# Kernel tuning notes

Measured on AMD Instinct MI355X. Metric: run time of the kernel, lower is better.

## Reference

```python
import jax, jax.numpy as jnp
import numpy as np

B, T, D = 256, 512, 256

def setup_inputs() -> dict:
    key = jax.random.key(0)
    k1, k2, k3, k4 = jax.random.split(key, 4)
    ip = jax.random.normal(k1, (B, T, D), dtype=jnp.float32)
    W = jax.random.normal(k2, (D, D), dtype=jnp.float32) * (1.0 / np.sqrt(D))
    b = jax.random.normal(k3, (D,), dtype=jnp.float32) * 0.05
    context = jax.random.normal(k4, (D, 1), dtype=jnp.float32) * 0.05
    return {"ip": ip, "W": W, "b": b, "context": context}

def reference(ip, W, b, context) -> jnp.ndarray:
    # linear -> tanh: [B, T, D]
    h = jnp.tanh(jnp.einsum("btd,ed->bte", ip, W) + b)
    # attention scores over words: [B, T]
    scores = jnp.einsum("btd,d->bt", h, context[:, 0])
    attn = jax.nn.softmax(scores, axis=1)
    # weighted sum over words -> sentence embeddings: [B, D]
    sent_embeds = jnp.einsum("bt,btd->bd", attn, ip)
    return sent_embeds
```

## Files before the change

### kernel.cpp

```cpp
#include <hip/hip_runtime.h>
#include <hip/hip_bf16.h>

#define NBATCH 256
#define NT 512
#define ND 256
#define NROWS (NBATCH * NT)

typedef __attribute__((ext_vector_type(8))) short short8;
typedef __attribute__((ext_vector_type(4))) float floatx4;

__device__ __forceinline__ unsigned short f2bf(float x) {
    unsigned int u = __float_as_uint(x);
    u += 0x7FFFu + ((u >> 16) & 1u);
    return (unsigned short)(u >> 16);
}

__global__ void __launch_bounds__(256) prep_kernel(
    const float* __restrict__ W, unsigned short* __restrict__ wf)
{
    int g  = blockIdx.x * 256 + threadIdx.x;
    int m  = g & 15, q = (g >> 4) & 3, s = (g >> 6) & 7, nb = g >> 9;
    const float* src = W + (nb * 16 + m) * ND + q * 8 + s * 32;
    float4 f0 = *(const float4*)src;
    float4 f1 = *(const float4*)(src + 4);
    short8 v;
    v[0] = (short)f2bf(f0.x); v[1] = (short)f2bf(f0.y);
    v[2] = (short)f2bf(f0.z); v[3] = (short)f2bf(f0.w);
    v[4] = (short)f2bf(f1.x); v[5] = (short)f2bf(f1.y);
    v[6] = (short)f2bf(f1.z); v[7] = (short)f2bf(f1.w);
    *(short8*)(wf + (long)g * 8) = v;
}

__global__ void __launch_bounds__(256, 4) scores_kernel(
    const float* __restrict__ ip,
    const unsigned short* __restrict__ wf,
    const float* __restrict__ bias,
    const float* __restrict__ ctx,
    float* __restrict__ scores)
{
    __shared__ __align__(16) char wsm[32768];
    short8* lds16 = (short8*)wsm;

    const int tid  = threadIdx.x;
    const int lane = tid & 63;
    const int wv   = tid >> 6;
    const int m    = lane & 15;
    const int q    = lane >> 4;
    const long row0 = (long)blockIdx.x * 64 + wv * 16;

    short8 a[8];
    {
        const float* ar = ip + (row0 + m) * ND + q * 8;
        float4 raw[8];
#pragma unroll
        for (int g = 0; g < 2; ++g) {
#pragma unroll
            for (int i = 0; i < 4; ++i) {
                raw[2 * i]     = *(const float4*)(ar + (4 * g + i) * 32);
                raw[2 * i + 1] = *(const float4*)(ar + (4 * g + i) * 32 + 4);
            }
#pragma unroll
            for (int i = 0; i < 4; ++i) {
                short8 v;
                v[0] = (short)f2bf(raw[2 * i].x); v[1] = (short)f2bf(raw[2 * i].y);
                v[2] = (short)f2bf(raw[2 * i].z); v[3] = (short)f2bf(raw[2 * i].w);
                v[4] = (short)f2bf(raw[2 * i + 1].x); v[5] = (short)f2bf(raw[2 * i + 1].y);
                v[6] = (short)f2bf(raw[2 * i + 1].z); v[7] = (short)f2bf(raw[2 * i + 1].w);
                a[4 * g + i] = v;
            }
        }
    }

    float sc[4] = {0.f, 0.f, 0.f, 0.f};
    const short8* wchunks = (const short8*)wf;

#pragma unroll 1
    for (int stage = 0; stage < 4; ++stage) {
        if (stage) __syncthreads();
#pragma unroll
        for (int u = 0; u < 8; ++u) {
            int c = u * 256 + tid;
            lds16[c] = wchunks[stage * 2048 + c];
        }
        __syncthreads();

#pragma unroll 1
        for (int nbl = 0; nbl < 4; ++nbl) {
            const int e = (stage * 4 + nbl) * 16 + m;
            const short8* wp = lds16 + nbl * 512 + lane;
            short8 w[8];
#pragma unroll
            for (int s = 0; s < 8; ++s) w[s] = wp[s * 64];
            floatx4 acc = {0.f, 0.f, 0.f, 0.f};
#pragma unroll
            for (int s = 0; s < 8; ++s)
                acc = __builtin_amdgcn_mfma_f32_16x16x32_bf16(a[s], w[s], acc, 0, 0, 0);
            const float be  = bias[e];
            const float ce  = ctx[e];
            const float ce2 = ce + ce;
#pragma unroll
            for (int r = 0; r < 4; ++r) {
                float x = acc[r] + be;
                float t = __builtin_amdgcn_rcpf(__expf(x + x) + 1.f);
                sc[r] = __builtin_fmaf(-ce2, t, sc[r] + ce);
            }
        }
    }

#pragma unroll
    for (int off = 8; off >= 1; off >>= 1) {
#pragma unroll
        for (int r = 0; r < 4; ++r)
            sc[r] += __shfl_xor(sc[r], off, 64);
    }
    if (m == 0) {
#pragma unroll
        for (int r = 0; r < 4; ++r)
            scores[row0 + q * 4 + r] = sc[r];
    }
}

__global__ void __launch_bounds__(256) wsum_kernel(
    const float* __restrict__ ip,
    const float* __restrict__ scores,
    float* __restrict__ out)
{
    __shared__ float attn_s[NT];
    __shared__ float red[8];
    __shared__ float partial[16][64];

    const int b  = blockIdx.x >> 2;
    const int dq = blockIdx.x & 3;
    const int tid  = threadIdx.x;
    const int lane = tid & 63;
    const int wv   = tid >> 6;

    float s0 = scores[(long)b * NT + tid];
    float s1 = scores[(long)b * NT + tid + 256];
    float mx = fmaxf(s0, s1);
#pragma unroll
    for (int off = 32; off >= 1; off >>= 1) mx = fmaxf(mx, __shfl_xor(mx, off, 64));
    if (lane == 0) red[wv] = mx;
    __syncthreads();
    mx = fmaxf(fmaxf(red[0], red[1]), fmaxf(red[2], red[3]));
    float e0 = __expf(s0 - mx), e1 = __expf(s1 - mx);
    float sm = e0 + e1;
#pragma unroll
    for (int off = 32; off >= 1; off >>= 1) sm += __shfl_xor(sm, off, 64);
    __syncthreads();
    if (lane == 0) red[4 + wv] = sm;
    __syncthreads();
    sm = red[4] + red[5] + red[6] + red[7];
    float inv = 1.f / sm;
    attn_s[tid]       = e0 * inv;
    attn_s[tid + 256] = e1 * inv;
    __syncthreads();

    const int dg = tid & 15;
    const int ts = tid >> 4;
    const float4* base = (const float4*)(ip + (long)b * NT * ND + dq * 64) + dg;
    float a0 = 0.f, a1 = 0.f, a2 = 0.f, a3 = 0.f;
#pragma unroll 8
    for (int t = ts * 32; t < ts * 32 + 32; ++t) {
        float w = attn_s[t];
        float4 v = base[t * 64];
        a0 += w * v.x; a1 += w * v.y; a2 += w * v.z; a3 += w * v.w;
    }
    partial[ts][dg * 4 + 0] = a0;
    partial[ts][dg * 4 + 1] = a1;
    partial[ts][dg * 4 + 2] = a2;
    partial[ts][dg * 4 + 3] = a3;
    __syncthreads();
    if (tid < 64) {
        float r = 0.f;
#pragma unroll
        for (int i = 0; i < 16; ++i) r += partial[i][tid];
        out[(long)b * ND + dq * 64 + tid] = r;
    }
}

extern "C" void kernel_launch(void* const* d_in, const int* in_sizes, int n_in,
                              void* d_out, int out_size, void* d_ws, size_t ws_size,
                              hipStream_t stream) {
    const float* ip   = (const float*)d_in[0];
    const float* W    = (const float*)d_in[1];
    const float* bias = (const float*)d_in[2];
    const float* ctx  = (const float*)d_in[3];

    unsigned short* wf = (unsigned short*)d_ws;
    float* scores = (float*)((char*)d_ws + ND * ND * sizeof(unsigned short));

    prep_kernel<<<32, 256, 0, stream>>>(W, wf);
    scores_kernel<<<NROWS / 64, 256, 0, stream>>>(ip, wf, bias, ctx, scores);
    wsum_kernel<<<NBATCH * 4, 256, 0, stream>>>(ip, scores, (float*)d_out);
}
```

Baseline: 232.9 us.

## Fuse weighted sum into scores kernel with split-softmax partials and combine pass

The separate weighted-sum kernel, which re-read all of ip from global memory, is folded into the scores kernel. Each 64-row block now computes a local max and exp-sum, weights its own rows (still cache-hot from the MFMA load) and writes a partial 256-vector. A small combine kernel merges the 8 chunks per batch with flash-style rescaling. This removes a full second pass over the 128 MB input. The cost is extra shared-memory syncs and reductions in the main kernel plus a partial-result buffer in workspace.

```diff
diff --git a/kernel.cpp b/kernel.cpp
--- a/kernel.cpp
+++ b/kernel.cpp
@@ -5,6 +5,7 @@
 #define NT 512
 #define ND 256
 #define NROWS (NBATCH * NT)
+#define NCHUNK (NROWS / 64)
 
 typedef __attribute__((ext_vector_type(8))) short short8;
 typedef __attribute__((ext_vector_type(4))) float floatx4;
@@ -31,14 +32,17 @@
     *(short8*)(wf + (long)g * 8) = v;
 }
 
-__global__ void __launch_bounds__(256, 4) scores_kernel(
+__global__ void __launch_bounds__(256, 4) fused_kernel(
     const float* __restrict__ ip,
     const unsigned short* __restrict__ wf,
     const float* __restrict__ bias,
     const float* __restrict__ ctx,
-    float* __restrict__ scores)
+    float* __restrict__ gpart,
+    float2* __restrict__ ml)
 {
     __shared__ __align__(16) char wsm[32768];
+    __shared__ float score_s[64];
+    __shared__ float w_s[64];
     short8* lds16 = (short8*)wsm;
 
     const int tid  = threadIdx.x;
@@ -116,67 +120,73 @@
     if (m == 0) {
 #pragma unroll
         for (int r = 0; r < 4; ++r)
-            scores[row0 + q * 4 + r] = sc[r];
-    }
-}
-
-__global__ void __launch_bounds__(256) wsum_kernel(
-    const float* __restrict__ ip,
-    const float* __restrict__ scores,
-    float* __restrict__ out)
-{
-    __shared__ float attn_s[NT];
-    __shared__ float red[8];
-    __shared__ float partial[16][64];
-
-    const int b  = blockIdx.x >> 2;
-    const int dq = blockIdx.x & 3;
-    const int tid  = threadIdx.x;
-    const int lane = tid & 63;
-    const int wv   = tid >> 6;
-
-    float s0 = scores[(long)b * NT + tid];
-    float s1 = scores[(long)b * NT + tid + 256];
-    float mx = fmaxf(s0, s1);
+            score_s[wv * 16 + q * 4 + r] = sc[r];
+    }
+    __syncthreads();
+
+    float s = score_s[lane];
+    float mx = s;
 #pragma unroll
     for (int off = 32; off >= 1; off >>= 1) mx = fmaxf(mx, __shfl_xor(mx, off, 64));
-    if (lane == 0) red[wv] = mx;
+    float w = __expf(s - mx);
+    float lsum = w;
+#pragma unroll
+    for (int off = 32; off >= 1; off >>= 1) lsum += __shfl_xor(lsum, off, 64);
+    if (wv == 0) w_s[lane] = w;
+    if (tid == 0) ml[blockIdx.x] = make_float2(mx, lsum);
     __syncthreads();
-    mx = fmaxf(fmaxf(red[0], red[1]), fmaxf(red[2], red[3]));
-    float e0 = __expf(s0 - mx), e1 = __expf(s1 - mx);
-    float sm = e0 + e1;
-#pragma unroll
-    for (int off = 32; off >= 1; off >>= 1) sm += __shfl_xor(sm, off, 64);
-    __syncthreads();
-    if (lane == 0) red[4 + wv] = sm;
-    __syncthreads();
-    sm = red[4] + red[5] + red[6] + red[7];
-    float inv = 1.f / sm;
-    attn_s[tid]       = e0 * inv;
-    attn_s[tid + 256] = e1 * inv;
-    __syncthreads();
-
-    const int dg = tid & 15;
-    const int ts = tid >> 4;
-    const float4* base = (const float4*)(ip + (long)b * NT * ND + dq * 64) + dg;
-    float a0 = 0.f, a1 = 0.f, a2 = 0.f, a3 = 0.f;
-#pragma unroll 8
-    for (int t = ts * 32; t < ts * 32 + 32; ++t) {
-        float w = attn_s[t];
-        float4 v = base[t * 64];
-        a0 += w * v.x; a1 += w * v.y; a2 += w * v.z; a3 += w * v.w;
-    }
-    partial[ts][dg * 4 + 0] = a0;
-    partial[ts][dg * 4 + 1] = a1;
-    partial[ts][dg * 4 + 2] = a2;
-    partial[ts][dg * 4 + 3] = a3;
+
+    const float4* base = (const float4*)ip + ((long)blockIdx.x * 64 + wv * 16) * 64 + lane;
+    float4 acc4 = {0.f, 0.f, 0.f, 0.f};
+#pragma unroll
+    for (int r = 0; r < 16; ++r) {
+        float wt = w_s[wv * 16 + r];
+        float4 v = base[(long)r * 64];
+        acc4.x += wt * v.x; acc4.y += wt * v.y;
+        acc4.z += wt * v.z; acc4.w += wt * v.w;
+    }
+    float4* part4 = (float4*)wsm;
+    part4[wv * 64 + lane] = acc4;
     __syncthreads();
     if (tid < 64) {
-        float r = 0.f;
-#pragma unroll
-        for (int i = 0; i < 16; ++i) r += partial[i][tid];
-        out[(long)b * ND + dq * 64 + tid] = r;
-    }
+        float4 r0 = part4[tid],       r1 = part4[64 + tid];
+        float4 r2 = part4[128 + tid], r3 = part4[192 + tid];
+        float4 o;
+        o.x = r0.x + r1.x + r2.x + r3.x;
+        o.y = r0.y + r1.y + r2.y + r3.y;
+        o.z = r0.z + r1.z + r2.z + r3.z;
+        o.w = r0.w + r1.w + r2.w + r3.w;
+        ((float4*)gpart)[(long)blockIdx.x * 64 + tid] = o;
+    }
+}
+
+__global__ void __launch_bounds__(256) combine_kernel(
+    const float4* __restrict__ gpart4,
+    const float2* __restrict__ ml,
+    float4* __restrict__ out4)
+{
+    const int b = blockIdx.x * 4 + (threadIdx.x >> 6);
+    const int c = threadIdx.x & 63;
+    const float2* mlb = ml + b * 8;
+    float mk[8], lk[8];
+#pragma unroll
+    for (int k = 0; k < 8; ++k) { float2 p = mlb[k]; mk[k] = p.x; lk[k] = p.y; }
+    float M = mk[0];
+#pragma unroll
+    for (int k = 1; k < 8; ++k) M = fmaxf(M, mk[k]);
+    float L = 0.f, f[8];
+#pragma unroll
+    for (int k = 0; k < 8; ++k) { f[k] = __expf(mk[k] - M); L += f[k] * lk[k]; }
+    float4 acc = {0.f, 0.f, 0.f, 0.f};
+#pragma unroll
+    for (int k = 0; k < 8; ++k) {
+        float4 v = gpart4[(long)(b * 8 + k) * 64 + c];
+        acc.x += f[k] * v.x; acc.y += f[k] * v.y;
+        acc.z += f[k] * v.z; acc.w += f[k] * v.w;
+    }
+    float inv = 1.f / L;
+    acc.x *= inv; acc.y *= inv; acc.z *= inv; acc.w *= inv;
+    out4[(long)b * 64 + c] = acc;
 }
 
 extern "C" void kernel_launch(void* const* d_in, const int* in_sizes, int n_in,
@@ -188,9 +198,10 @@
     const float* ctx  = (const float*)d_in[3];
 
     unsigned short* wf = (unsigned short*)d_ws;
-    float* scores = (float*)((char*)d_ws + ND * ND * sizeof(unsigned short));
+    float* gpart = (float*)((char*)d_ws + ND * ND * sizeof(unsigned short));
+    float2* ml   = (float2*)((char*)gpart + (long)NCHUNK * ND * sizeof(float));
 
     prep_kernel<<<32, 256, 0, stream>>>(W, wf);
-    scores_kernel<<<NROWS / 64, 256, 0, stream>>>(ip, wf, bias, ctx, scores);
-    wsum_kernel<<<NBATCH * 4, 256, 0, stream>>>(ip, scores, (float*)d_out);
-}
+    fused_kernel<<<NCHUNK, 256, 0, stream>>>(ip, wf, bias, ctx, gpart, ml);
+    combine_kernel<<<NBATCH / 4, 256, 0, stream>>>((const float4*)gpart, ml, (float4*)d_out);
+}
```

Measured after the change: 221.1 us. -5.0%, faster.

## Fuse scores, softmax and weighted sum into one per-batch kernel

Applied to the files above, without the earlier changes.

Replaces the separate scores and weighted-sum kernels with a single kernel per batch element. It runs 1024 threads and keeps the whole bf16 weight matrix resident in LDS, staged once per block instead of in four chunks per 64-row block. The softmax and weighted sum now happen in the same block right after the scores, so the scores round-trip through global memory goes away and the second read of `ip` is more likely to hit cache. In exchange there is only one large block per CU with heavy LDS use, which limits latency hiding, and the grid shrinks to 256 blocks.

```diff
diff --git a/kernel.cpp b/kernel.cpp
--- a/kernel.cpp
+++ b/kernel.cpp
@@ -4,7 +4,6 @@
 #define NBATCH 256
 #define NT 512
 #define ND 256
-#define NROWS (NBATCH * NT)
 
 typedef __attribute__((ext_vector_type(8))) short short8;
 typedef __attribute__((ext_vector_type(4))) float floatx4;
@@ -13,6 +12,15 @@
     unsigned int u = __float_as_uint(x);
     u += 0x7FFFu + ((u >> 16) & 1u);
     return (unsigned short)(u >> 16);
+}
+
+__device__ __forceinline__ short8 cvt8(float4 lo, float4 hi) {
+    short8 v;
+    v[0] = (short)f2bf(lo.x); v[1] = (short)f2bf(lo.y);
+    v[2] = (short)f2bf(lo.z); v[3] = (short)f2bf(lo.w);
+    v[4] = (short)f2bf(hi.x); v[5] = (short)f2bf(hi.y);
+    v[6] = (short)f2bf(hi.z); v[7] = (short)f2bf(hi.w);
+    return v;
 }
 
 __global__ void __launch_bounds__(256) prep_kernel(
@@ -23,159 +31,158 @@
     const float* src = W + (nb * 16 + m) * ND + q * 8 + s * 32;
     float4 f0 = *(const float4*)src;
     float4 f1 = *(const float4*)(src + 4);
-    short8 v;
-    v[0] = (short)f2bf(f0.x); v[1] = (short)f2bf(f0.y);
-    v[2] = (short)f2bf(f0.z); v[3] = (short)f2bf(f0.w);
-    v[4] = (short)f2bf(f1.x); v[5] = (short)f2bf(f1.y);
-    v[6] = (short)f2bf(f1.z); v[7] = (short)f2bf(f1.w);
-    *(short8*)(wf + (long)g * 8) = v;
-}
-
-__global__ void __launch_bounds__(256, 4) scores_kernel(
+    *(short8*)(wf + (long)g * 8) = cvt8(f0, f1);
+}
+
+__device__ __forceinline__ void score_tile(
+    const short8* __restrict__ wl, const short8 a[8],
+    const float* __restrict__ bias, const float* __restrict__ ctx,
+    int lane, int m, int q, float* __restrict__ score_dst)
+{
+    float sc[4] = {0.f, 0.f, 0.f, 0.f};
+#pragma unroll 1
+    for (int nb = 0; nb < 16; ++nb) {
+        const short8* wp = wl + nb * 512 + lane;
+        short8 w[4];
+#pragma unroll
+        for (int s = 0; s < 4; ++s) w[s] = wp[s * 64];
+        floatx4 acc = {0.f, 0.f, 0.f, 0.f};
+#pragma unroll
+        for (int s = 0; s < 4; ++s)
+            acc = __builtin_amdgcn_mfma_f32_16x16x32_bf16(a[s], w[s], acc, 0, 0, 0);
+#pragma unroll
+        for (int s = 0; s < 4; ++s) w[s] = wp[(s + 4) * 64];
+#pragma unroll
+        for (int s = 0; s < 4; ++s)
+            acc = __builtin_amdgcn_mfma_f32_16x16x32_bf16(a[s + 4], w[s], acc, 0, 0, 0);
+        const int e = nb * 16 + m;
+        const float be = bias[e];
+        const float ce = ctx[e];
+        const float ce2 = ce + ce;
+#pragma unroll
+        for (int r = 0; r < 4; ++r) {
+            float x = acc[r] + be;
+            float t = __builtin_amdgcn_rcpf(__expf(x + x) + 1.f);
+            sc[r] = __builtin_fmaf(-ce2, t, sc[r] + ce);
+        }
+    }
+#pragma unroll
+    for (int off = 8; off >= 1; off >>= 1)
+#pragma unroll
+        for (int r = 0; r < 4; ++r) sc[r] += __shfl_xor(sc[r], off, 64);
+    if (m == 0)
+#pragma unroll
+        for (int r = 0; r < 4; ++r) score_dst[q * 4 + r] = sc[r];
+}
+
+__global__ void __launch_bounds__(1024, 4) fused_kernel(
     const float* __restrict__ ip,
     const unsigned short* __restrict__ wf,
     const float* __restrict__ bias,
     const float* __restrict__ ctx,
-    float* __restrict__ scores)
+    float* __restrict__ out)
 {
-    __shared__ __align__(16) char wsm[32768];
-    short8* lds16 = (short8*)wsm;
+    __shared__ __align__(16) char wlds[131072];
+    __shared__ float score_s[NT];
+    __shared__ float w_s[NT];
+    __shared__ float red[16];
+    __shared__ __align__(16) float partial[16][ND];
 
     const int tid  = threadIdx.x;
     const int lane = tid & 63;
     const int wv   = tid >> 6;
     const int m    = lane & 15;
     const int q    = lane >> 4;
-    const long row0 = (long)blockIdx.x * 64 + wv * 16;
+    const long rowbase = (long)blockIdx.x * NT;
+    const short8* wl = (const short8*)wlds;
+
+    const float* ar1 = ip + (rowbase + wv * 16 + m) * ND + q * 8;
+    float4 raw[16];
+#pragma unroll
+    for (int s = 0; s < 8; ++s) {
+        raw[2 * s]     = *(const float4*)(ar1 + s * 32);
+        raw[2 * s + 1] = *(const float4*)(ar1 + s * 32 + 4);
+    }
+
+    {
+        short8* dst = (short8*)wlds;
+        const short8* src = (const short8*)wf;
+#pragma unroll 4
+        for (int u = 0; u < 8; ++u)
+            dst[u * 1024 + tid] = src[u * 1024 + tid];
+    }
 
     short8 a[8];
-    {
-        const float* ar = ip + (row0 + m) * ND + q * 8;
-        float4 raw[8];
-#pragma unroll
-        for (int g = 0; g < 2; ++g) {
-#pragma unroll
-            for (int i = 0; i < 4; ++i) {
-                raw[2 * i]     = *(const float4*)(ar + (4 * g + i) * 32);
-                raw[2 * i + 1] = *(const float4*)(ar + (4 * g + i) * 32 + 4);
-            }
-#pragma unroll
-            for (int i = 0; i < 4; ++i) {
-                short8 v;
-                v[0] = (short)f2bf(raw[2 * i].x); v[1] = (short)f2bf(raw[2 * i].y);
-                v[2] = (short)f2bf(raw[2 * i].z); v[3] = (short)f2bf(raw[2 * i].w);
-                v[4] = (short)f2bf(raw[2 * i + 1].x); v[5] = (short)f2bf(raw[2 * i + 1].y);
-                v[6] = (short)f2bf(raw[2 * i + 1].z); v[7] = (short)f2bf(raw[2 * i + 1].w);
-                a[4 * g + i] = v;
-            }
-        }
-    }
-
-    float sc[4] = {0.f, 0.f, 0.f, 0.f};
-    const short8* wchunks = (const short8*)wf;
-
-#pragma unroll 1
-    for (int stage = 0; stage < 4; ++stage) {
-        if (stage) __syncthreads();
-#pragma unroll
-        for (int u = 0; u < 8; ++u) {
-            int c = u * 256 + tid;
-            lds16[c] = wchunks[stage * 2048 + c];
-        }
-        __syncthreads();
-
-#pragma unroll 1
-        for (int nbl = 0; nbl < 4; ++nbl) {
-            const int e = (stage * 4 + nbl) * 16 + m;
-            const short8* wp = lds16 + nbl * 512 + lane;
-            short8 w[8];
-#pragma unroll
-            for (int s = 0; s < 8; ++s) w[s] = wp[s * 64];
-            floatx4 acc = {0.f, 0.f, 0.f, 0.f};
-#pragma unroll
-            for (int s = 0; s < 8; ++s)
-                acc = __builtin_amdgcn_mfma_f32_16x16x32_bf16(a[s], w[s], acc, 0, 0, 0);
-            const float be  = bias[e];
-            const float ce  = ctx[e];
-            const float ce2 = ce + ce;
-#pragma unroll
-            for (int r = 0; r < 4; ++r) {
-                float x = acc[r] + be;
-                float t = __builtin_amdgcn_rcpf(__expf(x + x) + 1.f);
-                sc[r] = __builtin_fmaf(-ce2, t, sc[r] + ce);
-            }
-        }
-    }
-
-#pragma unroll
-    for (int off = 8; off >= 1; off >>= 1) {
-#pragma unroll
-        for (int r = 0; r < 4; ++r)
-            sc[r] += __shfl_xor(sc[r], off, 64);
-    }
-    if (m == 0) {
-#pragma unroll
-        for (int r = 0; r < 4; ++r)
-            scores[row0 + q * 4 + r] = sc[r];
-    }
-}
-
-__global__ void __launch_bounds__(256) wsum_kernel(
-    const float* __restrict__ ip,
-    const float* __restrict__ scores,
-    float* __restrict__ out)
-{
-    __shared__ float attn_s[NT];
-    __shared__ float red[8];
-    __shared__ float partial[16][64];
-
-    const int b  = blockIdx.x >> 2;
-    const int dq = blockIdx.x & 3;
-    const int tid  = threadIdx.x;
-    const int lane = tid & 63;
-    const int wv   = tid >> 6;
-
-    float s0 = scores[(long)b * NT + tid];
-    float s1 = scores[(long)b * NT + tid + 256];
-    float mx = fmaxf(s0, s1);
-#pragma unroll
-    for (int off = 32; off >= 1; off >>= 1) mx = fmaxf(mx, __shfl_xor(mx, off, 64));
-    if (lane == 0) red[wv] = mx;
-    __syncthreads();
-    mx = fmaxf(fmaxf(red[0], red[1]), fmaxf(red[2], red[3]));
-    float e0 = __expf(s0 - mx), e1 = __expf(s1 - mx);
-    float sm = e0 + e1;
-#pragma unroll
-    for (int off = 32; off >= 1; off >>= 1) sm += __shfl_xor(sm, off, 64);
-    __syncthreads();
-    if (lane == 0) red[4 + wv] = sm;
-    __syncthreads();
-    sm = red[4] + red[5] + red[6] + red[7];
-    float inv = 1.f / sm;
-    attn_s[tid]       = e0 * inv;
-    attn_s[tid + 256] = e1 * inv;
-    __syncthreads();
-
-    const int dg = tid & 15;
-    const int ts = tid >> 4;
-    const float4* base = (const float4*)(ip + (long)b * NT * ND + dq * 64) + dg;
-    float a0 = 0.f, a1 = 0.f, a2 = 0.f, a3 = 0.f;
+#pragma unroll
+    for (int s = 0; s < 8; ++s) a[s] = cvt8(raw[2 * s], raw[2 * s + 1]);
+
+    __syncthreads();
+
+    const float* ar2 = ar1 + 256 * ND;
+    float4 rb[8];
+#pragma unroll
+    for (int s = 0; s < 4; ++s) {
+        rb[2 * s]     = *(const float4*)(ar2 + s * 32);
+        rb[2 * s + 1] = *(const float4*)(ar2 + s * 32 + 4);
+    }
+
+    score_tile(wl, a, bias, ctx, lane, m, q, score_s + wv * 16);
+
+#pragma unroll
+    for (int s = 0; s < 4; ++s) a[s] = cvt8(rb[2 * s], rb[2 * s + 1]);
+#pragma unroll
+    for (int s = 0; s < 4; ++s) {
+        rb[2 * s]     = *(const float4*)(ar2 + (s + 4) * 32);
+        rb[2 * s + 1] = *(const float4*)(ar2 + (s + 4) * 32 + 4);
+    }
+#pragma unroll
+    for (int s = 0; s < 4; ++s) a[s + 4] = cvt8(rb[2 * s], rb[2 * s + 1]);
+
+    score_tile(wl, a, bias, ctx, lane, m, q, score_s + 256 + wv * 16);
+
+    __syncthreads();
+
+    float sval = 0.f, e0 = 0.f;
+    if (wv < 8) {
+        sval = score_s[wv * 64 + lane];
+        float mx = sval;
+#pragma unroll
+        for (int off = 32; off >= 1; off >>= 1) mx = fmaxf(mx, __shfl_xor(mx, off, 64));
+        if (lane == 0) red[wv] = mx;
+    }
+    __syncthreads();
+    const float M = fmaxf(fmaxf(fmaxf(red[0], red[1]), fmaxf(red[2], red[3])),
+                          fmaxf(fmaxf(red[4], red[5]), fmaxf(red[6], red[7])));
+    if (wv < 8) {
+        e0 = __expf(sval - M);
+        float sm = e0;
+#pragma unroll
+        for (int off = 32; off >= 1; off >>= 1) sm += __shfl_xor(sm, off, 64);
+        if (lane == 0) red[8 + wv] = sm;
+    }
+    __syncthreads();
+    const float L = red[8] + red[9] + red[10] + red[11]
+                  + red[12] + red[13] + red[14] + red[15];
+    if (wv < 8) w_s[wv * 64 + lane] = e0 * (1.f / L);
+    __syncthreads();
+
+    const int prow = wv * 32;
+    const float4* base = (const float4*)(ip + (rowbase + prow) * ND) + lane;
+    float4 acc4 = {0.f, 0.f, 0.f, 0.f};
 #pragma unroll 8
-    for (int t = ts * 32; t < ts * 32 + 32; ++t) {
-        float w = attn_s[t];
-        float4 v = base[t * 64];
-        a0 += w * v.x; a1 += w * v.y; a2 += w * v.z; a3 += w * v.w;
-    }
-    partial[ts][dg * 4 + 0] = a0;
-    partial[ts][dg * 4 + 1] = a1;
-    partial[ts][dg * 4 + 2] = a2;
-    partial[ts][dg * 4 + 3] = a3;
-    __syncthreads();
-    if (tid < 64) {
+    for (int r = 0; r < 32; ++r) {
+        const float wt = w_s[prow + r];
+        const float4 v = base[(long)r * 64];
+        acc4.x += wt * v.x; acc4.y += wt * v.y;
+        acc4.z += wt * v.z; acc4.w += wt * v.w;
+    }
+    ((float4*)&partial[wv][0])[lane] = acc4;
+    __syncthreads();
+    if (tid < ND) {
         float r = 0.f;
 #pragma unroll
         for (int i = 0; i < 16; ++i) r += partial[i][tid];
-        out[(long)b * ND + dq * 64 + tid] = r;
+        out[(long)blockIdx.x * ND + tid] = r;
     }
 }
 
@@ -188,9 +195,7 @@
     const float* ctx  = (const float*)d_in[3];
 
     unsigned short* wf = (unsigned short*)d_ws;
-    float* scores = (float*)((char*)d_ws + ND * ND * sizeof(unsigned short));
 
     prep_kernel<<<32, 256, 0, stream>>>(W, wf);
-    scores_kernel<<<NROWS / 64, 256, 0, stream>>>(ip, wf, bias, ctx, scores);
-    wsum_kernel<<<NBATCH * 4, 256, 0, stream>>>(ip, scores, (float*)d_out);
-}
+    fused_kernel<<<NBATCH, 1024, 0, stream>>>(ip, wf, bias, ctx, (float*)d_out);
+}
```

Result: faster. 226.5 us (-2.7%).
